# Kernel optimization log

Measured on AMD Instinct MI355X. Metric: run time of the kernel, lower is better.

The kernel has to match this reference:

```python
import jax, jax.numpy as jnp
import numpy as np

B, T, D, H, DFF = 2, 2048, 1024, 16, 4096
DK = D // H
EPS = 1e-12
NEG = -1e9

def _ln(x, g, b):
    m = jnp.mean(x, axis=-1, keepdims=True)
    v = jnp.mean((x - m) ** 2, axis=-1, keepdims=True)
    return (x - m) / jnp.sqrt(v + EPS) * g + b

def setup_inputs() -> dict:
    key = jax.random.key(0)
    ks = jax.random.split(key, 8)
    s = 0.02
    return {
        "x": jax.random.normal(ks[0], (B, T, D), jnp.float32),
        "mask": jnp.ones((1, 1, T, T), jnp.int32),
        "wq": jax.random.normal(ks[1], (D, D), jnp.float32) * s,
        "bq": jnp.zeros((D,), jnp.float32),
        "wk": jax.random.normal(ks[2], (D, D), jnp.float32) * s,
        "bk": jnp.zeros((D,), jnp.float32),
        "wv": jax.random.normal(ks[3], (D, D), jnp.float32) * s,
        "bv": jnp.zeros((D,), jnp.float32),
        "wo": jax.random.normal(ks[4], (D, D), jnp.float32) * s,
        "bo": jnp.zeros((D,), jnp.float32),
        "w1": jax.random.normal(ks[5], (DFF, D), jnp.float32) * s,
        "b1": jnp.zeros((DFF,), jnp.float32),
        "w2": jax.random.normal(ks[6], (D, DFF), jnp.float32) * s,
        "b2": jnp.zeros((D,), jnp.float32),
        "g1": jnp.ones((D,), jnp.float32),
        "beta1": jnp.zeros((D,), jnp.float32),
        "g2": jnp.ones((D,), jnp.float32),
        "beta2": jnp.zeros((D,), jnp.float32),
    }

def reference(x, mask, wq, bq, wk, bk, wv, bv, wo, bo, w1, b1, w2, b2, g1, beta1, g2, beta2):
    # pre-norm (note: residual taken from ln1 output, faithful to source)
    xn = _ln(x, g1, beta1)
    # torch Linear: y = x @ W.T + b
    def proj(w, b):
        return (jnp.einsum('btd,ed->bte', xn, w) + b).reshape(B, T, H, DK).transpose(0, 2, 1, 3)
    q = proj(wq, bq)  # [B,H,T,DK]
    k = proj(wk, bk)
    v = proj(wv, bv)
    scores = jnp.einsum('bhqd,bhkd->bhqk', q, k) / jnp.sqrt(jnp.float32(DK))
    scores = jnp.where(mask == 0, jnp.float32(NEG), scores)
    weights = jax.nn.softmax(scores, axis=-1)  # dropout is identity in eval
    att = jnp.einsum('bhqk,bhkd->bhqd', weights, v)
    att = att.transpose(0, 2, 1, 3).reshape(B, T, D)
    h = jnp.einsum('btd,ed->bte', att, wo) + bo
    x = xn + h
    x = _ln(x, g2, beta2)
    ff = jax.nn.relu(jnp.einsum('btd,fd->btf', x, w1) + b1)
    ff = jnp.einsum('btf,df->btd', ff, w2) + b2
    return x + ff
```

## Files before the change

kernel.cpp:

```cpp
#include <hip/hip_runtime.h>

typedef unsigned short u16;
typedef __attribute__((ext_vector_type(8))) short short8;
typedef __attribute__((ext_vector_type(4))) float f32x4;
typedef __attribute__((ext_vector_type(4))) unsigned short u16x4;
typedef __attribute__((ext_vector_type(2))) unsigned int u32x2;

#define DEV static __device__ __forceinline__

DEV u16 f2b(float f) {
    unsigned int u = __builtin_bit_cast(unsigned int, f);
    u += 0x7FFFu + ((u >> 16) & 1u);
    return (u16)(u >> 16);
}
DEV float b2f(u16 v) {
    unsigned int u = ((unsigned int)v) << 16;
    return __builtin_bit_cast(float, u);
}
DEV void gload16(const void* g, void* l) {
    __builtin_amdgcn_global_load_lds((const __attribute__((address_space(1))) void*)g,
                                     (__attribute__((address_space(3))) void*)l,
                                     16, 0, 0);
}
DEV unsigned int cvt_pk(float lo, float hi) {
    unsigned int r;
    asm("v_cvt_pk_bf16_f32 %0, %1, %2" : "=v"(r) : "v"(lo), "v"(hi));
    return r;
}
#if __has_builtin(__builtin_amdgcn_exp2f)
DEV float ex2(float x) { return __builtin_amdgcn_exp2f(x); }
#else
DEV float ex2(float x) { return exp2f(x); }
#endif

static constexpr float KSCALE = 0.18033688011112042f;

__global__ __launch_bounds__(256) void cvt_all_k(
    const float* __restrict__ wq, const float* __restrict__ wk,
    const float* __restrict__ wv, const float* __restrict__ wo,
    const float* __restrict__ w1, const float* __restrict__ w2,
    u16* __restrict__ wqkv, u16* __restrict__ wo_b,
    u16* __restrict__ w1_b, u16* __restrict__ w2_b) {
    int bid = blockIdx.x;
    const float* s; u16* d; int off;
    if (bid < 1024)      { s = wq; d = wqkv;              off = bid; }
    else if (bid < 2048) { s = wk; d = wqkv + 1024*1024;  off = bid - 1024; }
    else if (bid < 3072) { s = wv; d = wqkv + 2048*1024;  off = bid - 2048; }
    else if (bid < 4096) { s = wo; d = wo_b;              off = bid - 3072; }
    else if (bid < 8192) { s = w1; d = w1_b;              off = bid - 4096; }
    else                 { s = w2; d = w2_b;              off = bid - 8192; }
    int i = off * 256 + threadIdx.x;
    float4 v = ((const float4*)s)[i];
    u16x4 o;
    o[0] = f2b(v.x); o[1] = f2b(v.y); o[2] = f2b(v.z); o[3] = f2b(v.w);
    ((u16x4*)d)[i] = o;
}

template <int INTYPE>
__global__ __launch_bounds__(256) void ln_k(const void* __restrict__ in,
                                            const float* __restrict__ g,
                                            const float* __restrict__ be,
                                            u16* __restrict__ outb) {
    int row = blockIdx.x;
    int t = threadIdx.x;
    float v[4];
    if constexpr (INTYPE == 0) {
        float4 x = ((const float4*)((const float*)in + (size_t)row * 1024))[t];
        v[0] = x.x; v[1] = x.y; v[2] = x.z; v[3] = x.w;
    } else {
        u16x4 x = ((const u16x4*)((const u16*)in + (size_t)row * 1024))[t];
#pragma unroll
        for (int i = 0; i < 4; i++) v[i] = b2f(x[i]);
    }
    float s = v[0] + v[1] + v[2] + v[3];
    float s2 = v[0] * v[0] + v[1] * v[1] + v[2] * v[2] + v[3] * v[3];
#pragma unroll
    for (int off = 1; off < 64; off <<= 1) {
        s += __shfl_xor(s, off);
        s2 += __shfl_xor(s2, off);
    }
    __shared__ float red[8];
    int wid = t >> 6, lane = t & 63;
    if (lane == 0) { red[wid] = s; red[4 + wid] = s2; }
    __syncthreads();
    float S = red[0] + red[1] + red[2] + red[3];
    float S2 = red[4] + red[5] + red[6] + red[7];
    float mean = S * (1.f / 1024.f);
    float var = fmaxf(S2 * (1.f / 1024.f) - mean * mean, 0.f);
    float rinv = rsqrtf(var + 1e-12f);
    float4 gv = ((const float4*)g)[t];
    float4 bv = ((const float4*)be)[t];
    u16x4 o;
    o[0] = f2b((v[0] - mean) * rinv * gv.x + bv.x);
    o[1] = f2b((v[1] - mean) * rinv * gv.y + bv.y);
    o[2] = f2b((v[2] - mean) * rinv * gv.z + bv.z);
    o[3] = f2b((v[3] - mean) * rinv * gv.w + bv.w);
    ((u16x4*)(outb + (size_t)row * 1024))[t] = o;
}

template <int EPI>
__global__ __launch_bounds__(512, 2) void gemm256(
    const u16* __restrict__ A, const u16* __restrict__ Bw,
    const float* __restrict__ b0, const float* __restrict__ b1,
    const float* __restrict__ b2, u16* __restrict__ outb,
    u16* __restrict__ kb, u16* __restrict__ vb, int M, int N, int K) {
    __shared__ u16 SB[3 * 16384];
    int tid = threadIdx.x, wid = tid >> 6, lane = tid & 63;
    int l15 = lane & 15, l4 = lane >> 4;
    int m0 = blockIdx.y * 256, n0 = blockIdx.x * 256;
    int wr = wid >> 2, wc = wid & 3;

    f32x4 acc[8][4] = {};

    int srow = tid >> 2;
    int sc = (tid & 3) * 8;
    const u16* Ag  = A  + (size_t)(m0 + srow) * K + sc;
    const u16* Ag2 = Ag + (size_t)128 * K;
    const u16* Bg  = Bw + (size_t)(n0 + srow) * K + sc;
    const u16* Bg2 = Bg + (size_t)128 * K;
    int ldst = wid * 1024;

    auto stageA = [&](int t, int bufi) {
        char* base = (char*)SB + bufi * 32768;
        size_t ko = (size_t)t * 32;
        gload16(Ag + ko, base + ldst);
        gload16(Ag2 + ko, base + 8192 + ldst);
    };
    auto stageB = [&](int t, int bufi) {
        char* base = (char*)SB + bufi * 32768 + 16384;
        size_t ko = (size_t)t * 32;
        gload16(Bg + ko, base + ldst);
        gload16(Bg2 + ko, base + 8192 + ldst);
    };

    const int NT = K >> 5;
    stageA(0, 0); stageB(0, 0);
    stageA(1, 1); stageB(1, 1);

    int cb = 0;
    for (int i = 0; i < NT; ++i) {
        if (i == NT - 1) asm volatile("s_waitcnt vmcnt(0)" ::: "memory");
        else             asm volatile("s_waitcnt vmcnt(4)" ::: "memory");
        __builtin_amdgcn_s_barrier();
        __builtin_amdgcn_sched_barrier(0);
        int sb = cb + 2; if (sb >= 3) sb -= 3;

        const u16* Abuf = SB + cb * 16384;
        const u16* Bbuf = Abuf + 8192;
        const u16* ap = &Abuf[(wr * 128 + l15) * 32 + l4 * 8];
        const u16* bp = &Bbuf[(wc * 64 + l15) * 32 + l4 * 8];
        short8 af[8], bfr[4];
#pragma unroll
        for (int x = 0; x < 4; x++) {
            af[x]  = *(const short8*)(ap + x * 512);
            bfr[x] = *(const short8*)(bp + x * 512);
        }
        if (i + 2 < NT) stageA(i + 2, sb);
#pragma unroll
        for (int x = 4; x < 8; x++) af[x] = *(const short8*)(ap + x * 512);
        if (i + 2 < NT) stageB(i + 2, sb);
        __builtin_amdgcn_s_setprio(1);
#pragma unroll
        for (int mi = 0; mi < 8; mi++)
#pragma unroll
            for (int ni = 0; ni < 4; ni++)
                acc[mi][ni] = __builtin_amdgcn_mfma_f32_16x16x32_bf16(
                    af[mi], bfr[ni], acc[mi][ni], 0, 0, 0);
        __builtin_amdgcn_s_setprio(0);
        cb = (cb == 2) ? 0 : cb + 1;
    }

#pragma unroll
    for (int mi = 0; mi < 8; mi++) {
#pragma unroll
        for (int ni = 0; ni < 4; ni++) {
            int n = n0 + wc * 64 + ni * 16 + l15;
            int mr = m0 + wr * 128 + mi * 16 + l4 * 4;
            if constexpr (EPI == 0) {
                int bidx = m0 >> 11;
                int t = mr & 2047;
                if (n0 < 1024) {
                    float bias = b0[n];
#pragma unroll
                    for (int r = 0; r < 4; r++)
                        outb[(size_t)(mr + r) * 1024 + n] =
                            f2b(acc[mi][ni][r] + bias);
                } else if (n0 < 2048) {
                    int nk = n - 1024, hh = nk >> 6, dk = nk & 63;
                    float bias = b1[nk];
                    size_t base = ((size_t)(bidx * 16 + hh) * 2048 + t) * 64 + dk;
#pragma unroll
                    for (int r = 0; r < 4; r++)
                        kb[base + (size_t)r * 64] =
                            f2b((acc[mi][ni][r] + bias) * KSCALE);
                } else {
                    int nv = n - 2048, hh = nv >> 6, dk = nv & 63;
                    int tile = t >> 5, kv = t & 31;
                    float bias = b2[nv];
                    u16x4 pk;
#pragma unroll
                    for (int r = 0; r < 4; r++) pk[r] = f2b(acc[mi][ni][r] + bias);
                    *(u16x4*)&vb[((((size_t)(bidx * 16 + hh) * 64 + tile) * 64 +
                                   dk) << 5) + kv] = pk;
                }
            } else {
                float bias = b0[n];
#pragma unroll
                for (int r = 0; r < 4; r++)
                    outb[(size_t)(mr + r) * N + n] =
                        f2b(fmaxf(acc[mi][ni][r] + bias, 0.f));
            }
        }
    }
}

template <int EPI, int BM>
__global__ __launch_bounds__(256) void gemm_bt(
    const u16* __restrict__ A, const u16* __restrict__ Bw,
    const float* __restrict__ b0, u16* __restrict__ outb,
    float* __restrict__ outf, const u16* __restrict__ res,
    int M, int N, int K) {
    constexpr int MFR = BM / 32;
    constexpr int BS = (BM + 128) * 32;
    __shared__ u16 SB[3 * BS];
    int tid = threadIdx.x, wid = tid >> 6, lane = tid & 63;
    int l15 = lane & 15, l4 = lane >> 4;
    int xw = blockIdx.y & 7;
    int yw = (blockIdx.y >> 3) * 8 + blockIdx.x;
    int m0 = yw * BM, n0 = xw * 128;
    int wr = wid >> 1, wc = wid & 1;

    f32x4 acc[MFR][4] = {};

    int srow = tid >> 2;
    int scol = (tid & 3) * 8;
    const u16* Ag  = A  + (size_t)(m0 + srow) * K + scol;
    const u16* Ag2 = Ag + (size_t)64 * K;
    const u16* Bg  = Bw + (size_t)(n0 + srow) * K + scol;
    const u16* Bg2 = Bg + (size_t)64 * K;
    int ldst = wid * 1024;

    auto stage = [&](int t, int bufi) {
        char* base = (char*)SB + (size_t)bufi * (BS * 2);
        size_t ko = (size_t)t * 32;
        gload16(Ag + ko, base + ldst);
        if constexpr (BM == 128) gload16(Ag2 + ko, base + 4096 + ldst);
        gload16(Bg + ko, base + BM * 64 + ldst);
        gload16(Bg2 + ko, base + BM * 64 + 4096 + ldst);
    };

    const int NT = K >> 5;
    stage(0, 0);
    stage(1, 1);

    int cb = 0;
    for (int i = 0; i < NT; ++i) {
        if (i == NT - 1) {
            asm volatile("s_waitcnt vmcnt(0)" ::: "memory");
        } else if constexpr (BM == 128) {
            asm volatile("s_waitcnt vmcnt(4)" ::: "memory");
        } else {
            asm volatile("s_waitcnt vmcnt(3)" ::: "memory");
        }
        __builtin_amdgcn_s_barrier();
        __builtin_amdgcn_sched_barrier(0);
        int sb = cb + 2; if (sb >= 3) sb -= 3;
        if (i + 2 < NT) stage(i + 2, sb);

        const u16* Abuf = SB + (size_t)cb * BS;
        const u16* Bbuf = Abuf + BM * 32;
        short8 af[MFR], bfr[4];
        const u16* ap = &Abuf[(wr * (BM / 2) + l15) * 32 + l4 * 8];
        const u16* bp = &Bbuf[(wc * 64 + l15) * 32 + l4 * 8];
#pragma unroll
        for (int i2 = 0; i2 < MFR; i2++) af[i2] = *(const short8*)(ap + i2 * 512);
#pragma unroll
        for (int i2 = 0; i2 < 4; i2++) bfr[i2] = *(const short8*)(bp + i2 * 512);
#pragma unroll
        for (int mi = 0; mi < MFR; mi++)
#pragma unroll
            for (int ni = 0; ni < 4; ni++)
                acc[mi][ni] = __builtin_amdgcn_mfma_f32_16x16x32_bf16(
                    af[mi], bfr[ni], acc[mi][ni], 0, 0, 0);
        cb = (cb == 2) ? 0 : cb + 1;
    }

    int mbase = m0 + wr * (BM / 2);
    int nbase = n0 + wc * 64;
#pragma unroll
    for (int mi = 0; mi < MFR; mi++) {
#pragma unroll
        for (int ni = 0; ni < 4; ni++) {
            int n = nbase + ni * 16 + l15;
            int mr = mbase + mi * 16 + l4 * 4;
            float bias = b0[n];
            if constexpr (EPI == 1) {
#pragma unroll
                for (int i = 0; i < 4; i++) {
                    size_t off = (size_t)(mr + i) * N + n;
                    outb[off] = f2b(acc[mi][ni][i] + bias + b2f(res[off]));
                }
            } else {
#pragma unroll
                for (int i = 0; i < 4; i++) {
                    size_t off = (size_t)(mr + i) * N + n;
                    outf[off] = acc[mi][ni][i] + bias + b2f(res[off]);
                }
            }
        }
    }
}

#define ATT_STAGE(KN, VN, TILE) do {                                          \
    int tl_ = ((TILE) + phase) & 31;                                          \
    gload16(Kg + tl_ * 2048, (char*)(KN) + ldst);                             \
    gload16(Vg + tl_ * 2048, (char*)(VN) + ldst);                             \
} while (0)

#define ATT_COMPUTE(KL, VL) do {                                              \
    f32x4 s_acc[2][2] = {};                                                   \
    {                                                                         \
        short8 kf[2][2];                                                      \
        _Pragma("unroll")                                                     \
        for (int kvt = 0; kvt < 2; kvt++) {                                   \
            int row = kvt * 16 + l15;                                         \
            kf[kvt][0] = *(const short8*)&(KL)[row * 64 + ((l4) ^ (row & 7)) * 8]; \
            kf[kvt][1] = *(const short8*)&(KL)[row * 64 + ((4 + l4) ^ (row & 7)) * 8]; \
        }                                                                     \
        __builtin_amdgcn_s_setprio(1);                                        \
        _Pragma("unroll")                                                     \
        for (int kvt = 0; kvt < 2; kvt++)                                     \
            _Pragma("unroll")                                                 \
            for (int qfi = 0; qfi < 2; qfi++) {                               \
                s_acc[kvt][qfi] = __builtin_amdgcn_mfma_f32_16x16x32_bf16(    \
                    kf[kvt][0], qf[qfi][0], s_acc[kvt][qfi], 0, 0, 0);        \
                s_acc[kvt][qfi] = __builtin_amdgcn_mfma_f32_16x16x32_bf16(    \
                    kf[kvt][1], qf[qfi][1], s_acc[kvt][qfi], 0, 0, 0);        \
            }                                                                 \
        __builtin_amdgcn_s_setprio(0);                                        \
    }                                                                         \
    _Pragma("unroll")                                                         \
    for (int qfi = 0; qfi < 2; qfi++) {                                       \
        char* Pq = Pw + qfi * 1152;                                           \
        _Pragma("unroll")                                                     \
        for (int kvt = 0; kvt < 2; kvt++) {                                   \
            u32x2 w;                                                          \
            w[0] = cvt_pk(ex2(s_acc[kvt][qfi][0]), ex2(s_acc[kvt][qfi][1]));  \
            w[1] = cvt_pk(ex2(s_acc[kvt][qfi][2]), ex2(s_acc[kvt][qfi][3]));  \
            *(u32x2*)(Pq + l15 * 72 + kvt * 32 + l4 * 8) = w;                 \
        }                                                                     \
    }                                                                         \
    {                                                                         \
        short8 pf[2], vf[4];                                                  \
        _Pragma("unroll")                                                     \
        for (int qfi = 0; qfi < 2; qfi++)                                     \
            pf[qfi] = *(const short8*)(Pw + qfi * 1152 + l15 * 72 + l4 * 16); \
        _Pragma("unroll")                                                     \
        for (int dt = 0; dt < 4; dt++) {                                      \
            int row = dt * 16 + l15;                                          \
            vf[dt] = *(const short8*)&(VL)[row * 32 + ((l4 ^ ((row >> 1) & 3))) * 8]; \
        }                                                                     \
        __builtin_amdgcn_s_setprio(1);                                        \
        _Pragma("unroll")                                                     \
        for (int qfi = 0; qfi < 2; qfi++)                                     \
            o_sum[qfi] = __builtin_amdgcn_mfma_f32_16x16x32_bf16(             \
                ones, pf[qfi], o_sum[qfi], 0, 0, 0);                          \
        _Pragma("unroll")                                                     \
        for (int dt = 0; dt < 4; dt++)                                        \
            _Pragma("unroll")                                                 \
            for (int qfi = 0; qfi < 2; qfi++)                                 \
                o_acc[dt][qfi] = __builtin_amdgcn_mfma_f32_16x16x32_bf16(     \
                    vf[dt], pf[qfi], o_acc[dt][qfi], 0, 0, 0);                \
        __builtin_amdgcn_s_setprio(0);                                        \
    }                                                                         \
} while (0)

#define ATT_ITER(CK, CV, NK, NV, TILE) do {                                   \
    asm volatile("s_waitcnt vmcnt(2)" ::: "memory");                          \
    __builtin_amdgcn_s_barrier();                                             \
    __builtin_amdgcn_sched_barrier(0);                                        \
    ATT_STAGE(NK, NV, TILE);                                                  \
    ATT_COMPUTE(CK, CV);                                                      \
} while (0)

__global__ __launch_bounds__(256, 4) void attn_k(const u16* __restrict__ qb,
                                                 const u16* __restrict__ kb,
                                                 const u16* __restrict__ vb,
                                                 u16* __restrict__ p0,
                                                 u16* __restrict__ p1,
                                                 float* __restrict__ s0,
                                                 float* __restrict__ s1) {
    __shared__ u16 K_lds[3][32 * 64];
    __shared__ u16 V_lds[3][64 * 32];
    __shared__ u16 P_lds[4][2][16 * 36];
    int tid = threadIdx.x, wid = tid >> 6, lane = tid & 63;
    int l15 = lane & 15, l4 = lane >> 4;
    int lin = blockIdx.x + 16 * blockIdx.y + 512 * blockIdx.z;
    int xcd = lin & 7, ii = lin >> 3;
    int pair = ((ii >> 4) << 3) + xcd;
    int qblk = ii & 15;
    int bh = pair & 31, z = pair >> 5;
    int b = bh >> 4, head = bh & 15;
    size_t boff = (size_t)b * 2048;
    int q0 = qblk * 128 + wid * 32;
    int phase = (qblk * 2) & 31;

    short8 qf[2][2];
#pragma unroll
    for (int qfi = 0; qfi < 2; qfi++) {
        const u16* qrow = qb + (boff + q0 + qfi * 16 + l15) * 1024 + head * 64 + l4 * 8;
        qf[qfi][0] = *(const short8*)(qrow);
        qf[qfi][1] = *(const short8*)(qrow + 32);
    }
    short8 ones;
#pragma unroll
    for (int j = 0; j < 8; j++) ones[j] = (short)0x3F80;

    f32x4 o_acc[4][2] = {};
    f32x4 o_sum[2] = {};
    char* Pw = (char*)&P_lds[wid][0][0];

    int krow = tid >> 3, kcs = (tid & 7) ^ (krow & 7);
    const u16* Kg = kb + ((size_t)bh * 2048 + z * 1024) * 64 + krow * 64 + kcs * 8;
    int vrow = tid >> 2, vcs = (tid & 3) ^ ((vrow >> 1) & 3);
    const u16* Vg = vb + ((size_t)bh * 64 + z * 32) * 2048 + vrow * 32 + vcs * 8;
    int ldst = wid * 1024;

    ATT_STAGE(&K_lds[0][0], &V_lds[0][0], 0);
    ATT_STAGE(&K_lds[1][0], &V_lds[1][0], 1);
    for (int g = 0; g < 10; g++) {
        ATT_ITER(&K_lds[0][0], &V_lds[0][0], &K_lds[2][0], &V_lds[2][0], 3 * g + 2);
        ATT_ITER(&K_lds[1][0], &V_lds[1][0], &K_lds[0][0], &V_lds[0][0], 3 * g + 3);
        ATT_ITER(&K_lds[2][0], &V_lds[2][0], &K_lds[1][0], &V_lds[1][0], 3 * g + 4);
    }
    asm volatile("s_waitcnt vmcnt(2)" ::: "memory");
    __builtin_amdgcn_s_barrier();
    __builtin_amdgcn_sched_barrier(0);
    ATT_COMPUTE(&K_lds[0][0], &V_lds[0][0]);
    asm volatile("s_waitcnt vmcnt(0)" ::: "memory");
    __builtin_amdgcn_s_barrier();
    __builtin_amdgcn_sched_barrier(0);
    ATT_COMPUTE(&K_lds[1][0], &V_lds[1][0]);

    u16* pz = z ? p1 : p0;
    float* sz = z ? s1 : s0;
#pragma unroll
    for (int qfi = 0; qfi < 2; qfi++) {
        int q = q0 + qfi * 16 + l15;
#pragma unroll
        for (int dt = 0; dt < 4; dt++) {
            u16x4 o;
#pragma unroll
            for (int r = 0; r < 4; r++) o[r] = f2b(o_acc[dt][qfi][r]);
            *(u16x4*)&pz[(boff + q) * 1024 + head * 64 + dt * 16 + l4 * 4] = o;
        }
        if (l4 == 0) sz[(boff + q) * 16 + head] = o_sum[qfi][0];
    }
}

__global__ __launch_bounds__(256) void attn_cmb(
    const u16* __restrict__ p0, const u16* __restrict__ p1,
    const float* __restrict__ s0, const float* __restrict__ s1,
    u16* __restrict__ att) {
    int idx = blockIdx.x * 256 + threadIdx.x;
    int row = idx >> 7, oct = idx & 127;
    int h = oct >> 3;
    float rs = 1.f / (s0[row * 16 + h] + s1[row * 16 + h]);
    size_t off = (size_t)row * 1024 + oct * 8;
    u16x4 a0 = ((const u16x4*)(p0 + off))[0];
    u16x4 a1 = ((const u16x4*)(p0 + off))[1];
    u16x4 c0 = ((const u16x4*)(p1 + off))[0];
    u16x4 c1 = ((const u16x4*)(p1 + off))[1];
    u16x4 o0, o1;
#pragma unroll
    for (int j = 0; j < 4; j++) {
        o0[j] = f2b((b2f(a0[j]) + b2f(c0[j])) * rs);
        o1[j] = f2b((b2f(a1[j]) + b2f(c1[j])) * rs);
    }
    ((u16x4*)(att + off))[0] = o0;
    ((u16x4*)(att + off))[1] = o1;
}

extern "C" void kernel_launch(void* const* d_in, const int* in_sizes, int n_in,
                              void* d_out, int out_size, void* d_ws, size_t ws_size,
                              hipStream_t stream) {
    (void)in_sizes; (void)n_in; (void)out_size; (void)ws_size;
    const float* x   = (const float*)d_in[0];
    const float* wq  = (const float*)d_in[2];
    const float* bq  = (const float*)d_in[3];
    const float* wk  = (const float*)d_in[4];
    const float* bk  = (const float*)d_in[5];
    const float* wv  = (const float*)d_in[6];
    const float* bv  = (const float*)d_in[7];
    const float* wo  = (const float*)d_in[8];
    const float* bo  = (const float*)d_in[9];
    const float* w1  = (const float*)d_in[10];
    const float* b1  = (const float*)d_in[11];
    const float* w2  = (const float*)d_in[12];
    const float* b2  = (const float*)d_in[13];
    const float* g1  = (const float*)d_in[14];
    const float* be1 = (const float*)d_in[15];
    const float* g2  = (const float*)d_in[16];
    const float* be2 = (const float*)d_in[17];
    float* out = (float*)d_out;

    char* ws = (char*)d_ws;
    u16* wqkv  = (u16*)(ws + (size_t)0);
    u16* wo_b  = (u16*)(ws + ((size_t)6  << 20));
    u16* w1_b  = (u16*)(ws + ((size_t)8  << 20));
    u16* w2_b  = (u16*)(ws + ((size_t)16 << 20));
    u16* xn_b  = (u16*)(ws + ((size_t)24 << 20));
    u16* x2_b  = (u16*)(ws + ((size_t)32 << 20));
    u16* x3_b  = (u16*)(ws + ((size_t)40 << 20));
    u16* q_b   = (u16*)(ws + ((size_t)48 << 20));
    u16* k_b   = (u16*)(ws + ((size_t)56 << 20));
    u16* v_b   = (u16*)(ws + ((size_t)64 << 20));
    u16* att_b = (u16*)(ws + ((size_t)72 << 20));
    float* s0_b = (float*)(ws + ((size_t)80 << 20));
    float* s1_b = (float*)(ws + ((size_t)80 << 20) + 262144);
    u16* ff_b  = (u16*)(ws + ((size_t)48 << 20));

    cvt_all_k<<<12288, 256, 0, stream>>>(wq, wk, wv, wo, w1, w2,
                                         wqkv, wo_b, w1_b, w2_b);
    ln_k<0><<<4096, 256, 0, stream>>>(x, g1, be1, xn_b);
    gemm256<0><<<dim3(12, 16), 512, 0, stream>>>(
        xn_b, wqkv, bq, bk, bv, q_b, k_b, v_b, 4096, 3072, 1024);
    attn_k<<<dim3(16, 32, 2), 256, 0, stream>>>(q_b, k_b, v_b, x2_b, x3_b,
                                                s0_b, s1_b);
    attn_cmb<<<2048, 256, 0, stream>>>(x2_b, x3_b, s0_b, s1_b, att_b);
    gemm_bt<1, 64><<<dim3(8, 64), 256, 0, stream>>>(
        att_b, wo_b, bo, x2_b, nullptr, xn_b, 4096, 1024, 1024);
    ln_k<1><<<4096, 256, 0, stream>>>(x2_b, g2, be2, x3_b);
    gemm256<2><<<dim3(16, 16), 512, 0, stream>>>(
        x3_b, w1_b, b1, nullptr, nullptr, ff_b, nullptr, nullptr, 4096, 4096, 1024);
    gemm_bt<3, 64><<<dim3(8, 64), 256, 0, stream>>>(
        ff_b, w2_b, b2, nullptr, out, x3_b, 4096, 1024, 4096);
}
```

Measured before the change: 235.2 us.

## Swizzle LDS layouts in GEMMs and deepen gemm_bt K-tile to 64

Adds an XOR swizzle on the 16-byte chunk index, applied both to the global-to-LDS staging addresses and to the fragment reads in gemm256, so that MFMA operand loads from shared memory avoid bank conflicts. gemm_bt gets a K-tile of 64 instead of 32 with an 8-chunk XOR swizzle, which halves the number of barrier-separated iterations and issues 6 loads per stage. It also raises wave priority around the MFMA block. The larger triple-buffered LDS footprint in gemm_bt may reduce occupancy.

```diff
diff --git a/kernel.cpp b/kernel.cpp
--- a/kernel.cpp
+++ b/kernel.cpp
@@ -113,10 +113,10 @@
     f32x4 acc[8][4] = {};
 
     int srow = tid >> 2;
-    int sc = (tid & 3) * 8;
-    const u16* Ag  = A  + (size_t)(m0 + srow) * K + sc;
+    int scs = (tid & 3) ^ ((srow >> 1) & 3);
+    const u16* Ag  = A  + (size_t)(m0 + srow) * K + scs * 8;
     const u16* Ag2 = Ag + (size_t)128 * K;
-    const u16* Bg  = Bw + (size_t)(n0 + srow) * K + sc;
+    const u16* Bg  = Bw + (size_t)(n0 + srow) * K + scs * 8;
     const u16* Bg2 = Bg + (size_t)128 * K;
     int ldst = wid * 1024;
 
@@ -137,6 +137,7 @@
     stageA(0, 0); stageB(0, 0);
     stageA(1, 1); stageB(1, 1);
 
+    int rch = (l4 ^ ((l15 >> 1) & 3)) * 8;
     int cb = 0;
     for (int i = 0; i < NT; ++i) {
         if (i == NT - 1) asm volatile("s_waitcnt vmcnt(0)" ::: "memory");
@@ -147,8 +148,8 @@
 
         const u16* Abuf = SB + cb * 16384;
         const u16* Bbuf = Abuf + 8192;
-        const u16* ap = &Abuf[(wr * 128 + l15) * 32 + l4 * 8];
-        const u16* bp = &Bbuf[(wc * 64 + l15) * 32 + l4 * 8];
+        const u16* ap = &Abuf[(wr * 128 + l15) * 32 + rch];
+        const u16* bp = &Bbuf[(wc * 64 + l15) * 32 + rch];
         short8 af[8], bfr[4];
 #pragma unroll
         for (int x = 0; x < 4; x++) {
@@ -214,81 +215,86 @@
     }
 }
 
-template <int EPI, int BM>
+template <int EPI>
 __global__ __launch_bounds__(256) void gemm_bt(
     const u16* __restrict__ A, const u16* __restrict__ Bw,
     const float* __restrict__ b0, u16* __restrict__ outb,
     float* __restrict__ outf, const u16* __restrict__ res,
     int M, int N, int K) {
-    constexpr int MFR = BM / 32;
-    constexpr int BS = (BM + 128) * 32;
+    constexpr int BS = 192 * 64;
     __shared__ u16 SB[3 * BS];
     int tid = threadIdx.x, wid = tid >> 6, lane = tid & 63;
     int l15 = lane & 15, l4 = lane >> 4;
     int xw = blockIdx.y & 7;
     int yw = (blockIdx.y >> 3) * 8 + blockIdx.x;
-    int m0 = yw * BM, n0 = xw * 128;
+    int m0 = yw * 64, n0 = xw * 128;
     int wr = wid >> 1, wc = wid & 1;
 
-    f32x4 acc[MFR][4] = {};
-
-    int srow = tid >> 2;
-    int scol = (tid & 3) * 8;
-    const u16* Ag  = A  + (size_t)(m0 + srow) * K + scol;
-    const u16* Ag2 = Ag + (size_t)64 * K;
-    const u16* Bg  = Bw + (size_t)(n0 + srow) * K + scol;
-    const u16* Bg2 = Bg + (size_t)64 * K;
+    f32x4 acc[2][4] = {};
+
+    int srow = tid >> 3;
+    int scs = (tid & 7) ^ (srow & 7);
+    const u16* Ag = A  + (size_t)(m0 + srow) * K + scs * 8;
+    const u16* Bg = Bw + (size_t)(n0 + srow) * K + scs * 8;
     int ldst = wid * 1024;
 
     auto stage = [&](int t, int bufi) {
         char* base = (char*)SB + (size_t)bufi * (BS * 2);
-        size_t ko = (size_t)t * 32;
-        gload16(Ag + ko, base + ldst);
-        if constexpr (BM == 128) gload16(Ag2 + ko, base + 4096 + ldst);
-        gload16(Bg + ko, base + BM * 64 + ldst);
-        gload16(Bg2 + ko, base + BM * 64 + 4096 + ldst);
+        size_t ko = (size_t)t * 64;
+        gload16(Ag + ko,              base + ldst);
+        gload16(Ag + 32 * (size_t)K + ko, base + 4096 + ldst);
+        gload16(Bg + ko,              base + 8192 + ldst);
+        gload16(Bg + 32 * (size_t)K + ko, base + 12288 + ldst);
+        gload16(Bg + 64 * (size_t)K + ko, base + 16384 + ldst);
+        gload16(Bg + 96 * (size_t)K + ko, base + 20480 + ldst);
     };
 
-    const int NT = K >> 5;
+    const int NT = K >> 6;
     stage(0, 0);
     stage(1, 1);
 
+    int swz = l15 & 7;
     int cb = 0;
     for (int i = 0; i < NT; ++i) {
-        if (i == NT - 1) {
-            asm volatile("s_waitcnt vmcnt(0)" ::: "memory");
-        } else if constexpr (BM == 128) {
-            asm volatile("s_waitcnt vmcnt(4)" ::: "memory");
-        } else {
-            asm volatile("s_waitcnt vmcnt(3)" ::: "memory");
-        }
+        if (i == NT - 1) asm volatile("s_waitcnt vmcnt(0)" ::: "memory");
+        else             asm volatile("s_waitcnt vmcnt(6)" ::: "memory");
         __builtin_amdgcn_s_barrier();
         __builtin_amdgcn_sched_barrier(0);
         int sb = cb + 2; if (sb >= 3) sb -= 3;
         if (i + 2 < NT) stage(i + 2, sb);
 
         const u16* Abuf = SB + (size_t)cb * BS;
-        const u16* Bbuf = Abuf + BM * 32;
-        short8 af[MFR], bfr[4];
-        const u16* ap = &Abuf[(wr * (BM / 2) + l15) * 32 + l4 * 8];
-        const u16* bp = &Bbuf[(wc * 64 + l15) * 32 + l4 * 8];
-#pragma unroll
-        for (int i2 = 0; i2 < MFR; i2++) af[i2] = *(const short8*)(ap + i2 * 512);
-#pragma unroll
-        for (int i2 = 0; i2 < 4; i2++) bfr[i2] = *(const short8*)(bp + i2 * 512);
-#pragma unroll
-        for (int mi = 0; mi < MFR; mi++)
-#pragma unroll
-            for (int ni = 0; ni < 4; ni++)
-                acc[mi][ni] = __builtin_amdgcn_mfma_f32_16x16x32_bf16(
-                    af[mi], bfr[ni], acc[mi][ni], 0, 0, 0);
+        const u16* Bbuf = Abuf + 4096;
+        short8 af[2][2], bfr[4][2];
+#pragma unroll
+        for (int mi = 0; mi < 2; mi++)
+#pragma unroll
+            for (int kc = 0; kc < 2; kc++)
+                af[mi][kc] = *(const short8*)&Abuf[(wr * 32 + mi * 16 + l15) * 64 +
+                                                   ((kc * 4 + l4) ^ swz) * 8];
+#pragma unroll
+        for (int ni = 0; ni < 4; ni++)
+#pragma unroll
+            for (int kc = 0; kc < 2; kc++)
+                bfr[ni][kc] = *(const short8*)&Bbuf[(wc * 64 + ni * 16 + l15) * 64 +
+                                                    ((kc * 4 + l4) ^ swz) * 8];
+        __builtin_amdgcn_s_setprio(1);
+#pragma unroll
+        for (int kc = 0; kc < 2; kc++)
+#pragma unroll
+            for (int mi = 0; mi < 2; mi++)
+#pragma unroll
+                for (int ni = 0; ni < 4; ni++)
+                    acc[mi][ni] = __builtin_amdgcn_mfma_f32_16x16x32_bf16(
+                        af[mi][kc], bfr[ni][kc], acc[mi][ni], 0, 0, 0);
+        __builtin_amdgcn_s_setprio(0);
         cb = (cb == 2) ? 0 : cb + 1;
     }
 
-    int mbase = m0 + wr * (BM / 2);
+    int mbase = m0 + wr * 32;
     int nbase = n0 + wc * 64;
 #pragma unroll
-    for (int mi = 0; mi < MFR; mi++) {
+    for (int mi = 0; mi < 2; mi++) {
 #pragma unroll
         for (int ni = 0; ni < 4; ni++) {
             int n = nbase + ni * 16 + l15;
@@ -528,11 +534,11 @@
     attn_k<<<dim3(16, 32, 2), 256, 0, stream>>>(q_b, k_b, v_b, x2_b, x3_b,
                                                 s0_b, s1_b);
     attn_cmb<<<2048, 256, 0, stream>>>(x2_b, x3_b, s0_b, s1_b, att_b);
-    gemm_bt<1, 64><<<dim3(8, 64), 256, 0, stream>>>(
+    gemm_bt<1><<<dim3(8, 64), 256, 0, stream>>>(
         att_b, wo_b, bo, x2_b, nullptr, xn_b, 4096, 1024, 1024);
     ln_k<1><<<4096, 256, 0, stream>>>(x2_b, g2, be2, x3_b);
     gemm256<2><<<dim3(16, 16), 512, 0, stream>>>(
         x3_b, w1_b, b1, nullptr, nullptr, ff_b, nullptr, nullptr, 4096, 4096, 1024);
-    gemm_bt<3, 64><<<dim3(8, 64), 256, 0, stream>>>(
+    gemm_bt<3><<<dim3(8, 64), 256, 0, stream>>>(
         ff_b, w2_b, b2, nullptr, out, x3_b, 4096, 1024, 4096);
 }
```

Measured after the change: 218.4 us. 1.08x faster.
